# Optimization experiments

Measured on AMD Instinct MI355X. Metric: run time of the kernel, lower is better.

Reference implementation:

```python
import jax, jax.numpy as jnp
import numpy as np
import math

SQ, SK, B, NP, HN = 2048, 2048, 2, 16, 128
LAYER_NUM = 1  # coeff
NORM_FACTOR = math.sqrt(2048 / 16) * LAYER_NUM  # sqrt(HIDDEN/HEADS) * coeff
SCALE = float(LAYER_NUM)  # MLSASoftmax scale


def setup_inputs() -> dict:
    key = jax.random.key(0)
    kq, kk, kv = jax.random.split(key, 3)
    query_layer = jax.random.normal(kq, (SQ, B, NP, HN), dtype=jnp.float32)
    key_layer = jax.random.normal(kk, (SK, B, NP, HN), dtype=jnp.float32)
    value_layer = jax.random.normal(kv, (SK, B, NP, HN), dtype=jnp.float32)
    # Causal mask: True = masked, shape [b, 1, sq, sk] (broadcasts over heads)
    causal = jnp.triu(jnp.ones((SQ, SK), dtype=bool), k=1)
    attention_mask = jnp.broadcast_to(causal[None, None], (B, 1, SQ, SK))
    return {
        "query_layer": query_layer,
        "key_layer": key_layer,
        "value_layer": value_layer,
        "attention_mask": attention_mask,
    }


def reference(query_layer, key_layer, value_layer, attention_mask):
    # scores[b,n,s,t] = (Q . K) / norm_factor, then * coeff in softmax
    scores = jnp.einsum("sbnh,tbnh->bnst", query_layer, key_layer) / NORM_FACTOR
    scores = scores * SCALE
    scores = jnp.where(attention_mask, jnp.float32(-10000.0), scores)
    # Module computes exp/sum WITHOUT max-subtraction; replicate exactly.
    exp_mo = jnp.exp(scores)
    denomi = jnp.sum(exp_mo, axis=-1, keepdims=True)  # [b, np, sq, 1]
    probs = exp_mo / denomi
    # dropout is identity in eval / for deterministic baseline
    ctx = jnp.einsum("bnst,tbnh->sbnh", probs, value_layer)  # [sq, b, np, hn]
    sq, b, n, h = ctx.shape
    context_layer = ctx.reshape(sq, b, n * h)
    return (context_layer, denomi)
```

## Files before the change

### kernel.cpp

```cpp
#include <hip/hip_runtime.h>
#include <hip/hip_bf16.h>
#include <stdint.h>

typedef __attribute__((ext_vector_type(8))) short short8;
typedef __attribute__((ext_vector_type(8))) unsigned short ushort8;
typedef __attribute__((ext_vector_type(4))) float f32x4;
typedef __attribute__((ext_vector_type(4))) int int4v;

#define NHEAD 32
#define SEQ   2048
#define HN    128

static constexpr float INV_NORM = 0.08838834764831845f;

__device__ __forceinline__ unsigned short f2bf(float f) {
  union { float f; unsigned u; } v; v.f = f;
  unsigned r = v.u + 0x7fffu + ((v.u >> 16) & 1u);
  return (unsigned short)(r >> 16);
}

__device__ __forceinline__ f32x4 mfma16(short8 a, short8 b, f32x4 c) {
  return __builtin_amdgcn_mfma_f32_16x16x32_bf16(a, b, c, 0, 0, 0);
}

__device__ __forceinline__ void gl_lds16(const void* g, void* l) {
  __builtin_amdgcn_global_load_lds(
      (const __attribute__((address_space(1))) unsigned int*)g,
      (__attribute__((address_space(3))) unsigned int*)l, 16, 0, 0);
}

__global__ __launch_bounds__(256) void prep_kv(const float* __restrict__ K,
                                               const float* __restrict__ V,
                                               unsigned short* __restrict__ kswz,
                                               unsigned short* __restrict__ vT) {
  __shared__ unsigned short lds[128 * 136];
  int bid = blockIdx.x;
  int tid = threadIdx.x;
  if (bid < 4096) {
    int idx = bid * 256 + tid;
    int cl = idx & 15;
    int t  = (idx >> 4) & 2047;
    int bn = idx >> 15;
    const float4* src = (const float4*)(K + ((size_t)t * 32 + bn) * 128 + cl * 8);
    float4 a = src[0], b = src[1];
    ushort8 o;
    o[0]=f2bf(a.x); o[1]=f2bf(a.y); o[2]=f2bf(a.z); o[3]=f2bf(a.w);
    o[4]=f2bf(b.x); o[5]=f2bf(b.y); o[6]=f2bf(b.z); o[7]=f2bf(b.w);
    *(ushort8*)(kswz + ((size_t)bn * 2048 + t) * 128 + ((cl ^ (t & 7)) * 8)) = o;
  } else {
    int vb = bid - 4096;
    int bn = vb >> 4;
    int t0 = (vb & 15) << 7;
    int r = tid >> 1, h0 = (tid & 1) * 64;
    const float* src = V + ((size_t)(t0 + r) * 32 + bn) * 128 + h0;
#pragma unroll
    for (int j = 0; j < 8; ++j) {
      float4 a = *(const float4*)(src + j * 8);
      float4 b = *(const float4*)(src + j * 8 + 4);
      ushort8 o;
      o[0]=f2bf(a.x); o[1]=f2bf(a.y); o[2]=f2bf(a.z); o[3]=f2bf(a.w);
      o[4]=f2bf(b.x); o[5]=f2bf(b.y); o[6]=f2bf(b.z); o[7]=f2bf(b.w);
      *(ushort8*)&lds[r * 136 + h0 + j * 8] = o;
    }
    __syncthreads();
    int h = tid >> 1, ts = (tid & 1) * 64;
    unsigned short tmp[64];
#pragma unroll
    for (int j = 0; j < 64; ++j) {
      int p = j & 31;
      int tloc = ((p >> 3) & 3) * 4 + ((p >> 2) & 1) * 16 + (p & 3);
      tmp[j] = lds[(ts + (j & 32) + tloc) * 136 + h];
    }
    ushort8* dst = (ushort8*)(vT + ((size_t)bn * 128 + h) * 2048 + t0 + ts);
#pragma unroll
    for (int j = 0; j < 8; ++j) dst[j] = *(ushort8*)&tmp[j * 8];
  }
}

__device__ __forceinline__ void read_kf(const char* kb, int base, int l15, int hi,
                                        short8 (&kf)[2][4]) {
  int xr = (l15 & 7) << 4;
#pragma unroll
  for (int nt = 0; nt < 2; ++nt) {
    const char* krow = kb + (base + nt * 16 + l15) * 256;
#pragma unroll
    for (int kk = 0; kk < 4; ++kk)
      kf[nt][kk] = *(const short8*)(krow + (((kk * 4 + hi) * 16) ^ xr));
  }
}

__device__ __forceinline__ void read_vf(const char* vbh, int l15, int hi,
                                        short8 (&vf)[8]) {
#pragma unroll
  for (int ht = 0; ht < 8; ++ht)
    vf[ht] = *(const short8*)(vbh + (ht * 16 + l15) * 64 +
                              ((((l15 >> 1) + hi) & 3) * 16));
}

__device__ __forceinline__ short8 packp(const float (&e)[8], float& da) {
  da += ((e[0] + e[1]) + (e[2] + e[3])) + ((e[4] + e[5]) + (e[6] + e[7]));
  unsigned w0, w1, w2, w3;
  asm("v_cvt_pk_bf16_f32 %0, %1, %2" : "=v"(w0) : "v"(e[0]), "v"(e[1]));
  asm("v_cvt_pk_bf16_f32 %0, %1, %2" : "=v"(w1) : "v"(e[2]), "v"(e[3]));
  asm("v_cvt_pk_bf16_f32 %0, %1, %2" : "=v"(w2) : "v"(e[4]), "v"(e[5]));
  asm("v_cvt_pk_bf16_f32 %0, %1, %2" : "=v"(w3) : "v"(e[6]), "v"(e[7]));
  union { int4v u; short8 s; } pk;
  pk.u = (int4v){(int)w0, (int)w1, (int)w2, (int)w3};
  return pk.s;
}

__device__ __forceinline__ short8 softp_m(const f32x4 (&sv)[2], int t0h, int qbase,
                                          int l15, int hi, float& da) {
  float e[8];
#pragma unroll
  for (int nt = 0; nt < 2; ++nt)
#pragma unroll
    for (int i = 0; i < 4; ++i) {
      float x = __expf(sv[nt][i]);
      int kv = t0h + nt * 16 + hi * 4 + i;
      e[nt * 4 + i] = (kv <= qbase + l15) ? x : 0.0f;
    }
  return packp(e, da);
}

__device__ __forceinline__ short8 softp_u(const f32x4 (&sv)[2], float& da) {
  float e[8];
#pragma unroll
  for (int nt = 0; nt < 2; ++nt)
#pragma unroll
    for (int i = 0; i < 4; ++i)
      e[nt * 4 + i] = __expf(sv[nt][i]);
  return packp(e, da);
}

__device__ __forceinline__ void half_tile(
    const char* kb, const char* vbh, int halfbase, int t0h, int q0, int q1,
    int l15, int hi, const short8 (&qf)[2][4],
    f32x4 (&acc)[2][8], float (&dacc)[2]) {
  f32x4 zz = {0.f, 0.f, 0.f, 0.f};
  short8 kf[2][4];
  read_kf(kb, halfbase, l15, hi, kf);
  f32x4 s0[2] = {zz, zz}, s1[2] = {zz, zz};
  __builtin_amdgcn_s_setprio(1);
#pragma unroll
  for (int nt = 0; nt < 2; ++nt)
#pragma unroll
    for (int kk = 0; kk < 4; ++kk) {
      s0[nt] = mfma16(kf[nt][kk], qf[0][kk], s0[nt]);
      s1[nt] = mfma16(kf[nt][kk], qf[1][kk], s1[nt]);
    }
  __builtin_amdgcn_s_setprio(0);
  short8 vf[8];
  read_vf(vbh, l15, hi, vf);
  bool m0 = (t0h + 31 > q0);
  short8 p0 = m0 ? softp_m(s0, t0h, q0, l15, hi, dacc[0]) : softp_u(s0, dacc[0]);
  bool m1 = (t0h + 31 > q1);
  short8 p1 = m1 ? softp_m(s1, t0h, q1, l15, hi, dacc[1]) : softp_u(s1, dacc[1]);
  __builtin_amdgcn_s_setprio(1);
#pragma unroll
  for (int ht = 0; ht < 8; ++ht) {
    acc[0][ht] = mfma16(p0, vf[ht], acc[0][ht]);
    acc[1][ht] = mfma16(p1, vf[ht], acc[1][ht]);
  }
  __builtin_amdgcn_s_setprio(0);
}

__global__ __launch_bounds__(256, 2) void attn_main(const float* __restrict__ Q,
                                                    const unsigned short* __restrict__ kswz,
                                                    const unsigned short* __restrict__ vT,
                                                    float* __restrict__ out) {
  __shared__ char smem[65536];
  int tid = threadIdx.x;
  int lane = tid & 63;
  int w = tid >> 6;
  int l15 = lane & 15;
  int hi = lane >> 4;

  int bid = blockIdx.x;
  int bn = bid & 31;
  int z = bid >> 5;
  int qt = (z < 8) ? (15 - z) : (z - 8);
  int qb0 = qt * 128 + w * 32;
  int qb1 = qb0 + 16;
  int ntile = 2 * qt + 2;

  short8 qf[2][4];
#pragma unroll
  for (int qs = 0; qs < 2; ++qs) {
    int qbase = qs ? qb1 : qb0;
    const float* qrow = Q + ((size_t)(qbase + l15) * 32 + bn) * 128;
#pragma unroll
    for (int kk = 0; kk < 4; ++kk) {
      float4 a = *(const float4*)(qrow + kk * 32 + hi * 8);
      float4 b = *(const float4*)(qrow + kk * 32 + hi * 8 + 4);
      short8 o;
      o[0]=(short)f2bf(a.x*INV_NORM); o[1]=(short)f2bf(a.y*INV_NORM);
      o[2]=(short)f2bf(a.z*INV_NORM); o[3]=(short)f2bf(a.w*INV_NORM);
      o[4]=(short)f2bf(b.x*INV_NORM); o[5]=(short)f2bf(b.y*INV_NORM);
      o[6]=(short)f2bf(b.z*INV_NORM); o[7]=(short)f2bf(b.w*INV_NORM);
      qf[qs][kk] = o;
    }
  }

  f32x4 zz = {0.f, 0.f, 0.f, 0.f};
  f32x4 acc[2][8];
#pragma unroll
  for (int qs = 0; qs < 2; ++qs)
#pragma unroll
    for (int ht = 0; ht < 8; ++ht) acc[qs][ht] = zz;
  float dacc[2] = {0.f, 0.f};

  const char* kg = (const char*)(kswz + (size_t)bn * 2048 * 128);
  const char* vg = (const char*)(vT + (size_t)bn * 128 * 2048);

  auto stage = [&](int buf, int t0) {
    const char* ksrc = kg + (size_t)t0 * 256;
    char* kl = smem + buf * 16384;
    int c = w * 64 + lane;
#pragma unroll
    for (int rr = 0; rr < 4; ++rr)
      gl_lds16(ksrc + (size_t)(c + rr * 256) * 16, kl + (c + rr * 256) * 16);
    char* vl = smem + 32768 + buf * 16384;
#pragma unroll
    for (int s = 0; s < 2; ++s)
#pragma unroll
      for (int rr = 0; rr < 2; ++rr) {
        int c2 = c + rr * 256;
        int h = c2 >> 2, sp = c2 & 3;
        int sl = (sp - (h >> 1)) & 3;
        gl_lds16(vg + (size_t)h * 4096 + (t0 + s * 32) * 2 + sl * 16,
                 vl + s * 8192 + c2 * 16);
      }
  };

  asm volatile("s_waitcnt vmcnt(0)" ::: "memory");
  stage(0, 0);

  int cur = 0;
  for (int it = 0; it < ntile; ++it) {
    int t0 = it * 64;
    asm volatile("s_waitcnt vmcnt(0)" ::: "memory");
    __builtin_amdgcn_s_barrier();
    if (it + 1 < ntile) stage(cur ^ 1, t0 + 64);

    const char* kb = smem + cur * 16384;
    const char* vb = smem + 32768 + cur * 16384;
#pragma unroll
    for (int half = 0; half < 2; ++half) {
      int t0h = t0 + half * 32;
      if (t0h <= qb0)
        half_tile(kb, vb + half * 8192, half * 32, t0h, qb0, qb1,
                  l15, hi, qf, acc, dacc);
    }
    cur ^= 1;
  }

#pragma unroll
  for (int qs = 0; qs < 2; ++qs) {
    float d = dacc[qs];
    d += __shfl_xor(d, 16);
    d += __shfl_xor(d, 32);
    dacc[qs] = d;
  }
  float* dn = out + 8388608;
  if (hi == 0) {
    dn[(size_t)bn * 2048 + qb0 + l15] = dacc[0];
    dn[(size_t)bn * 2048 + qb1 + l15] = dacc[1];
  }
  float inv0[4], inv1[4];
#pragma unroll
  for (int i = 0; i < 4; ++i) {
    inv0[i] = __builtin_amdgcn_rcpf(__shfl(dacc[0], hi * 4 + i));
    inv1[i] = __builtin_amdgcn_rcpf(__shfl(dacc[1], hi * 4 + i));
  }

#pragma unroll
  for (int qs = 0; qs < 2; ++qs) {
    int qbase = qs ? qb1 : qb0;
#pragma unroll
    for (int i = 0; i < 4; ++i) {
      float inv = qs ? inv1[i] : inv0[i];
      float* orow = out + (size_t)(qbase + hi * 4 + i) * 4096 + bn * 128 + l15;
#pragma unroll
      for (int ht = 0; ht < 8; ++ht)
        orow[ht * 16] = acc[qs][ht][i] * inv;
    }
  }
}

extern "C" void kernel_launch(void* const* d_in, const int* in_sizes, int n_in,
                              void* d_out, int out_size, void* d_ws, size_t ws_size,
                              hipStream_t stream) {
  const float* Q = (const float*)d_in[0];
  const float* K = (const float*)d_in[1];
  const float* V = (const float*)d_in[2];
  float* out = (float*)d_out;

  unsigned short* kswz = (unsigned short*)d_ws;
  unsigned short* vT   = kswz + (size_t)NHEAD * SEQ * HN;

  prep_kv<<<4608, 256, 0, stream>>>(K, V, kswz, vT);
  attn_main<<<512, 256, 0, stream>>>(Q, kswz, vT, out);
}
```

Before: 85.43 us.

## Split KV sequence across two wave groups per block with LDS reduction

Doubles the block to 512 threads and gives each group of four waves alternating 32-key tiles, so each wave set handles half the KV loop for the same query rows. Partial accumulators and denominators from the second group are reduced through shared memory at the end. K fragments are now read from LDS before the next stage is issued, to overlap the read with prefetch. This adds a large LDS reduction (16 f32x4 per thread) and extra barriers, and may raise register pressure under launch_bounds(512,2).

New measurement: 93.25 us. +9.1%, slower.

```diff
diff --git a/kernel.cpp b/kernel.cpp
--- a/kernel.cpp
+++ b/kernel.cpp
@@ -77,12 +77,12 @@
   }
 }
 
-__device__ __forceinline__ void read_kf(const char* kb, int base, int l15, int hi,
+__device__ __forceinline__ void read_kf(const char* kb, int l15, int hi,
                                         short8 (&kf)[2][4]) {
   int xr = (l15 & 7) << 4;
 #pragma unroll
   for (int nt = 0; nt < 2; ++nt) {
-    const char* krow = kb + (base + nt * 16 + l15) * 256;
+    const char* krow = kb + (nt * 16 + l15) * 256;
 #pragma unroll
     for (int kk = 0; kk < 4; ++kk)
       kf[nt][kk] = *(const short8*)(krow + (((kk * 4 + hi) * 16) ^ xr));
@@ -133,46 +133,16 @@
   return packp(e, da);
 }
 
-__device__ __forceinline__ void half_tile(
-    const char* kb, const char* vbh, int halfbase, int t0h, int q0, int q1,
-    int l15, int hi, const short8 (&qf)[2][4],
-    f32x4 (&acc)[2][8], float (&dacc)[2]) {
-  f32x4 zz = {0.f, 0.f, 0.f, 0.f};
-  short8 kf[2][4];
-  read_kf(kb, halfbase, l15, hi, kf);
-  f32x4 s0[2] = {zz, zz}, s1[2] = {zz, zz};
-  __builtin_amdgcn_s_setprio(1);
-#pragma unroll
-  for (int nt = 0; nt < 2; ++nt)
-#pragma unroll
-    for (int kk = 0; kk < 4; ++kk) {
-      s0[nt] = mfma16(kf[nt][kk], qf[0][kk], s0[nt]);
-      s1[nt] = mfma16(kf[nt][kk], qf[1][kk], s1[nt]);
-    }
-  __builtin_amdgcn_s_setprio(0);
-  short8 vf[8];
-  read_vf(vbh, l15, hi, vf);
-  bool m0 = (t0h + 31 > q0);
-  short8 p0 = m0 ? softp_m(s0, t0h, q0, l15, hi, dacc[0]) : softp_u(s0, dacc[0]);
-  bool m1 = (t0h + 31 > q1);
-  short8 p1 = m1 ? softp_m(s1, t0h, q1, l15, hi, dacc[1]) : softp_u(s1, dacc[1]);
-  __builtin_amdgcn_s_setprio(1);
-#pragma unroll
-  for (int ht = 0; ht < 8; ++ht) {
-    acc[0][ht] = mfma16(p0, vf[ht], acc[0][ht]);
-    acc[1][ht] = mfma16(p1, vf[ht], acc[1][ht]);
-  }
-  __builtin_amdgcn_s_setprio(0);
-}
-
-__global__ __launch_bounds__(256, 2) void attn_main(const float* __restrict__ Q,
+__global__ __launch_bounds__(512, 2) void attn_main(const float* __restrict__ Q,
                                                     const unsigned short* __restrict__ kswz,
                                                     const unsigned short* __restrict__ vT,
                                                     float* __restrict__ out) {
   __shared__ char smem[65536];
   int tid = threadIdx.x;
   int lane = tid & 63;
-  int w = tid >> 6;
+  int w8 = tid >> 6;
+  int w = w8 & 3;
+  int sid = w8 >> 2;
   int l15 = lane & 15;
   int hi = lane >> 4;
 
@@ -182,7 +152,7 @@
   int qt = (z < 8) ? (15 - z) : (z - 8);
   int qb0 = qt * 128 + w * 32;
   int qb1 = qb0 + 16;
-  int ntile = 2 * qt + 2;
+  int nIt = 2 * (qt + 1);
 
   short8 qf[2][4];
 #pragma unroll
@@ -213,47 +183,100 @@
   const char* kg = (const char*)(kswz + (size_t)bn * 2048 * 128);
   const char* vg = (const char*)(vT + (size_t)bn * 128 * 2048);
 
-  auto stage = [&](int buf, int t0) {
-    const char* ksrc = kg + (size_t)t0 * 256;
-    char* kl = smem + buf * 16384;
+  char* kbase = smem + sid * 16384;
+  char* vbase = smem + 32768 + sid * 16384;
+
+  auto stage = [&](int buf, int t) {
+    const char* ksrc = kg + (size_t)t * 8192;
+    char* kl = kbase + buf * 8192;
     int c = w * 64 + lane;
 #pragma unroll
-    for (int rr = 0; rr < 4; ++rr)
+    for (int rr = 0; rr < 2; ++rr)
       gl_lds16(ksrc + (size_t)(c + rr * 256) * 16, kl + (c + rr * 256) * 16);
-    char* vl = smem + 32768 + buf * 16384;
-#pragma unroll
-    for (int s = 0; s < 2; ++s)
-#pragma unroll
-      for (int rr = 0; rr < 2; ++rr) {
-        int c2 = c + rr * 256;
-        int h = c2 >> 2, sp = c2 & 3;
-        int sl = (sp - (h >> 1)) & 3;
-        gl_lds16(vg + (size_t)h * 4096 + (t0 + s * 32) * 2 + sl * 16,
-                 vl + s * 8192 + c2 * 16);
-      }
+    char* vl = vbase + buf * 8192;
+#pragma unroll
+    for (int rr = 0; rr < 2; ++rr) {
+      int c2 = c + rr * 256;
+      int h = c2 >> 2, sp = c2 & 3;
+      int sl = (sp - (h >> 1)) & 3;
+      gl_lds16(vg + (size_t)h * 4096 + (size_t)t * 64 + sl * 16,
+               vl + c2 * 16);
+    }
   };
 
   asm volatile("s_waitcnt vmcnt(0)" ::: "memory");
-  stage(0, 0);
+  stage(0, sid);
 
   int cur = 0;
-  for (int it = 0; it < ntile; ++it) {
-    int t0 = it * 64;
+  for (int it = 0; it < nIt; ++it) {
+    int t = it * 2 + sid;
+    int t0h = t * 32;
     asm volatile("s_waitcnt vmcnt(0)" ::: "memory");
     __builtin_amdgcn_s_barrier();
-    if (it + 1 < ntile) stage(cur ^ 1, t0 + 64);
-
-    const char* kb = smem + cur * 16384;
-    const char* vb = smem + 32768 + cur * 16384;
-#pragma unroll
-    for (int half = 0; half < 2; ++half) {
-      int t0h = t0 + half * 32;
-      if (t0h <= qb0)
-        half_tile(kb, vb + half * 8192, half * 32, t0h, qb0, qb1,
-                  l15, hi, qf, acc, dacc);
+
+    const char* kb = kbase + cur * 8192;
+    const char* vbh = vbase + cur * 8192;
+    bool act = (t0h <= qb0 + 31);
+
+    short8 kf[2][4];
+    if (act) read_kf(kb, l15, hi, kf);
+    if (it + 1 < nIt) stage(cur ^ 1, t + 2);
+
+    if (act) {
+      f32x4 s0[2] = {zz, zz}, s1[2] = {zz, zz};
+      __builtin_amdgcn_s_setprio(1);
+#pragma unroll
+      for (int nt = 0; nt < 2; ++nt)
+#pragma unroll
+        for (int kk = 0; kk < 4; ++kk) {
+          s0[nt] = mfma16(kf[nt][kk], qf[0][kk], s0[nt]);
+          s1[nt] = mfma16(kf[nt][kk], qf[1][kk], s1[nt]);
+        }
+      __builtin_amdgcn_s_setprio(0);
+      short8 vf[8];
+      read_vf(vbh, l15, hi, vf);
+      bool m0 = (t0h + 31 > qb0);
+      short8 p0 = m0 ? softp_m(s0, t0h, qb0, l15, hi, dacc[0])
+                     : softp_u(s0, dacc[0]);
+      bool m1 = (t0h + 31 > qb1);
+      short8 p1 = m1 ? softp_m(s1, t0h, qb1, l15, hi, dacc[1])
+                     : softp_u(s1, dacc[1]);
+      __builtin_amdgcn_s_setprio(1);
+#pragma unroll
+      for (int ht = 0; ht < 8; ++ht) {
+        acc[0][ht] = mfma16(p0, vf[ht], acc[0][ht]);
+        acc[1][ht] = mfma16(p1, vf[ht], acc[1][ht]);
+      }
+      __builtin_amdgcn_s_setprio(0);
     }
     cur ^= 1;
   }
+
+  __syncthreads();
+  int sl = w * 64 + lane;
+  float* dsm = (float*)smem;
+  if (sid == 1) { dsm[sl] = dacc[0]; dsm[256 + sl] = dacc[1]; }
+  __syncthreads();
+  if (sid == 0) { dacc[0] += dsm[sl]; dacc[1] += dsm[256 + sl]; }
+  __syncthreads();
+  f32x4* accsm = (f32x4*)smem;
+  if (sid == 1) {
+#pragma unroll
+    for (int qs = 0; qs < 2; ++qs)
+#pragma unroll
+      for (int ht = 0; ht < 8; ++ht)
+        accsm[(qs * 8 + ht) * 256 + sl] = acc[qs][ht];
+  }
+  __syncthreads();
+  if (sid == 1) return;
+#pragma unroll
+  for (int qs = 0; qs < 2; ++qs)
+#pragma unroll
+    for (int ht = 0; ht < 8; ++ht) {
+      f32x4 o = accsm[(qs * 8 + ht) * 256 + sl];
+      acc[qs][ht][0] += o[0]; acc[qs][ht][1] += o[1];
+      acc[qs][ht][2] += o[2]; acc[qs][ht][3] += o[3];
+    }
 
 #pragma unroll
   for (int qs = 0; qs < 2; ++qs) {
@@ -300,5 +323,5 @@
   unsigned short* vT   = kswz + (size_t)NHEAD * SEQ * HN;
 
   prep_kv<<<4608, 256, 0, stream>>>(K, V, kswz, vT);
-  attn_main<<<512, 256, 0, stream>>>(Q, kswz, vT, out);
-}
+  attn_main<<<512, 512, 0, stream>>>(Q, kswz, vT, out);
+}
```
